# Kernel optimization log

Hardware: AMD Instinct MI355X
Metric: run time of the kernel (lower is better)

The kernel has to match this reference:

```python
import jax, jax.numpy as jnp
import numpy as np

N = 100000
F = 128
H = 128
E = 3200000


def setup_inputs() -> dict:
    key = jax.random.key(0)
    ks = jax.random.split(key, 12)
    s = 1.0 / np.sqrt(F)
    return {
        "x": jax.random.normal(ks[0], (N, F), jnp.float32),
        "edge_weight": jax.random.uniform(ks[1], (E,), jnp.float32),
        "p": jax.random.normal(ks[2], (F,), jnp.float32) * s,
        "w_ih": jax.random.normal(ks[3], (3 * F, F), jnp.float32) * s,
        "w_hh": jax.random.normal(ks[4], (3 * F, F), jnp.float32) * s,
        "b_ih": jax.random.normal(ks[5], (3 * F,), jnp.float32) * s,
        "b_hh": jax.random.normal(ks[6], (3 * F,), jnp.float32) * s,
        "w0": jax.random.normal(ks[7], (F, F), jnp.float32) * s,
        "w_lin": jax.random.normal(ks[8], (H, F), jnp.float32) * s,
        "b_lin": jax.random.normal(ks[9], (H,), jnp.float32) * s,
        "edge_index": jax.random.randint(ks[10], (2, E), 0, N, jnp.int64),
    }


def _evolve_gcnh(x, edge_index, edge_weight, p, w_ih, w_hh, b_ih, b_hh, w0):
    n_nodes, f = x.shape
    # --- TopKPooling: keep k = f nodes by learned projection score ---
    score = jnp.tanh((x @ p) / jnp.linalg.norm(p))  # [N]
    top_scores, idx = jax.lax.top_k(score, f)
    x_tilde = x[idx] * top_scores[:, None]  # [F, F]
    # --- single GRU step (batch=F, input=F): hidden state = GCN weight ---
    gi = x_tilde @ w_ih.T + b_ih  # [F, 3F]
    gh = w0 @ w_hh.T + b_hh       # [F, 3F]
    i_r, i_z, i_n = jnp.split(gi, 3, axis=-1)
    h_r, h_z, h_n = jnp.split(gh, 3, axis=-1)
    r = jax.nn.sigmoid(i_r + h_r)
    z = jax.nn.sigmoid(i_z + h_z)
    n = jnp.tanh(i_n + r * h_n)
    W = (1.0 - z) * n + z * w0  # evolved weight [F, F]
    # --- GCNConv with fixed W: sym-normalized sparse aggregation ---
    src, dst = edge_index[0], edge_index[1]
    loop = jnp.arange(n_nodes)
    src = jnp.concatenate([src, loop])
    dst = jnp.concatenate([dst, loop])
    ew = jnp.concatenate([edge_weight, jnp.ones((n_nodes,), x.dtype)])
    deg = jax.ops.segment_sum(ew, dst, num_segments=n_nodes)
    dinv = jnp.where(deg > 0, jax.lax.rsqrt(deg), 0.0)
    norm = dinv[src] * ew * dinv[dst]  # [E+N]
    xw = x @ W  # [N, F]
    out = jax.ops.segment_sum(norm[:, None] * xw[src], dst, num_segments=n_nodes)
    return out


def reference(x, edge_weight, p, w_ih, w_hh, b_ih, b_hh, w0, w_lin, b_lin, edge_index):
    h = _evolve_gcnh(x, edge_index, edge_weight, p, w_ih, w_hh, b_ih, b_hh, w0)
    h = jax.nn.relu(h)
    return h @ w_lin.T + b_lin
```

## Files before the change

kernel.cpp:

```cpp
#include <hip/hip_runtime.h>
#include <stdint.h>

#define FD 128
#define CAP 4096
#define PSH 8
#define NPART_MAX 512
#define NBLK1 256

static inline size_t alignup256(size_t x) { return (x + 255) & ~(size_t)255; }

struct EdgeP { int s; float w; };

typedef __attribute__((ext_vector_type(4))) float f32x4;
typedef __attribute__((ext_vector_type(8))) short bf16x8;

__device__ __forceinline__ unsigned short f32_to_bf16(float f) {
  unsigned u = __float_as_uint(f);
  u += 0x7fffu + ((u >> 16) & 1u);
  return (unsigned short)(u >> 16);
}
__device__ __forceinline__ float bf16lo(unsigned pair) {
  return __uint_as_float(pair << 16);
}
__device__ __forceinline__ float bf16hi(unsigned pair) {
  return __uint_as_float(pair & 0xffff0000u);
}
__device__ __forceinline__ unsigned pack_bf16(float a, float b) {
  return ((unsigned)f32_to_bf16(b) << 16) | (unsigned)f32_to_bf16(a);
}
__device__ __forceinline__ unsigned mono32(float f) {
  unsigned u = __float_as_uint(f);
  return (u & 0x80000000u) ? ~u : (u | 0x80000000u);
}
__device__ __forceinline__ unsigned long long mono64(double d) {
  unsigned long long b = (unsigned long long)__double_as_longlong(d);
  return (b & 0x8000000000000000ULL) ? ~b : (b | 0x8000000000000000ULL);
}

__global__ void score_pack(const float* __restrict__ x, const float* __restrict__ p,
                           double* __restrict__ dvals, unsigned* __restrict__ hist,
                           unsigned short* __restrict__ xb, unsigned* __restrict__ cnt, int N)
{
  int gid = blockIdx.x * blockDim.x + threadIdx.x;
  if (gid == 0) *cnt = 0u;
  int wid = gid >> 6, lane = threadIdx.x & 63;
  int nw = (gridDim.x * blockDim.x) >> 6;
  double p0 = (double)p[lane * 2], p1 = (double)p[lane * 2 + 1];
  for (int n = wid; n < N; n += nw) {
    float2 xv = *(const float2*)(x + (size_t)n * FD + lane * 2);
    unsigned pk = pack_bf16(xv.x, xv.y);
    *(unsigned*)(xb + (size_t)n * FD + lane * 2) = pk;
    double s = (double)xv.x * p0 + (double)xv.y * p1;
    #pragma unroll
    for (int o = 32; o > 0; o >>= 1) s += __shfl_down(s, o, 64);
    if (lane == 0) {
      dvals[n] = s;
      unsigned u = mono32((float)s);
      atomicAdd(&hist[u >> 16], 1u);
    }
  }
}

__global__ void find_thresh(const unsigned* __restrict__ hist, unsigned* __restrict__ Bthr)
{
  __shared__ unsigned part[1024];
  int t = threadIdx.x;
  unsigned s = 0;
  for (int i = 0; i < 64; i++) s += hist[t * 64 + i];
  part[t] = s;
  __syncthreads();
  if (t == 0) {
    unsigned cum = 0;
    int chunk = 1023;
    for (; chunk >= 0; chunk--) {
      if (cum + part[chunk] >= 128u) break;
      cum += part[chunk];
    }
    unsigned B = 0;
    if (chunk >= 0) {
      int b = chunk * 64 + 63;
      for (; b >= chunk * 64; b--) {
        cum += hist[b];
        if (cum >= 128u) break;
      }
      B = (unsigned)b;
    }
    *Bthr = B;
  }
}

__global__ void compact_kernel(const double* __restrict__ dvals, const unsigned* __restrict__ Bthr,
                               unsigned long long* __restrict__ ckey, unsigned* __restrict__ cidx,
                               unsigned* __restrict__ cnt, int N)
{
  int i = blockIdx.x * blockDim.x + threadIdx.x;
  if (i >= N) return;
  unsigned B = *Bthr;
  double d = dvals[i];
  unsigned u = mono32((float)d);
  if ((u >> 16) >= B) {
    unsigned pos = atomicAdd(cnt, 1u);
    if (pos < CAP) {
      ckey[pos] = ~mono64(d);
      cidx[pos] = (unsigned)i;
    }
  }
}

__global__ void topk_sort(const double* __restrict__ dvals, const float* __restrict__ p,
                          const unsigned* __restrict__ cnt,
                          const unsigned long long* __restrict__ ckey, const unsigned* __restrict__ cidx,
                          unsigned* __restrict__ sel_idx, float* __restrict__ sel_ts)
{
  __shared__ unsigned long long k[CAP];
  __shared__ unsigned id[CAP];
  __shared__ double red[128];
  __shared__ double pn_sh;
  int t = threadIdx.x;
  unsigned C = *cnt;
  if (C > CAP) C = CAP;
  int S = 128;
  while (S < (int)C) S <<= 1;
  for (int i = t; i < S; i += 1024) {
    if (i < (int)C) { k[i] = ckey[i]; id[i] = cidx[i]; }
    else            { k[i] = ~0ULL;   id[i] = 0xFFFFFFFFu; }
  }
  __syncthreads();
  for (int kk = 2; kk <= S; kk <<= 1) {
    for (int j = kk >> 1; j > 0; j >>= 1) {
      for (int i = t; i < S; i += 1024) {
        int q = i ^ j;
        if (q > i) {
          bool up = ((i & kk) == 0);
          bool g = (k[i] > k[q]) || (k[i] == k[q] && id[i] > id[q]);
          if (g == up) {
            unsigned long long tk = k[i]; k[i] = k[q]; k[q] = tk;
            unsigned ti = id[i]; id[i] = id[q]; id[q] = ti;
          }
        }
      }
      __syncthreads();
    }
  }
  if (t < 128) { double v = (double)p[t]; red[t] = v * v; }
  __syncthreads();
  if (t == 0) {
    double s = 0.0;
    for (int i = 0; i < 128; i++) s += red[i];
    pn_sh = sqrt(s);
  }
  __syncthreads();
  if (t < 128) {
    unsigned n = id[t];
    sel_idx[t] = n;
    sel_ts[t] = (float)tanh(dvals[n] / pn_sh);
  }
}

__global__ void transpose3(const float* __restrict__ w_ih, const float* __restrict__ w_hh,
                           const float* __restrict__ w_lin, float* __restrict__ w_ihT,
                           float* __restrict__ w_hhT, unsigned short* __restrict__ wlb)
{
  int b = blockIdx.x, c = threadIdx.x;
  if (b < 384)      w_ihT[(size_t)c * 384 + b]         = w_ih[(size_t)b * 128 + c];
  else if (b < 768) w_hhT[(size_t)c * 384 + (b - 384)] = w_hh[(size_t)(b - 384) * 128 + c];
  else              wlb[(size_t)(b - 768) * 128 + c]   = f32_to_bf16(w_lin[(size_t)(b - 768) * 128 + c]);
}

__global__ void gru_evolve(const float* __restrict__ x, const unsigned* __restrict__ sel_idx,
                           const float* __restrict__ sel_ts,
                           const float* __restrict__ w_ihT, const float* __restrict__ w_hhT,
                           const float* __restrict__ b_ih, const float* __restrict__ b_hh,
                           const float* __restrict__ w0, unsigned short* __restrict__ WbT)
{
  __shared__ float xt[FD], w0r[FD];
  int i = blockIdx.x, j = threadIdx.x;
  unsigned n = sel_idx[i];
  float ts = sel_ts[i];
  xt[j]  = x[(size_t)n * FD + j] * ts;
  w0r[j] = w0[i * FD + j];
  __syncthreads();
  float gir = b_ih[j], giz = b_ih[128 + j], gin = b_ih[256 + j];
  float ghr = b_hh[j], ghz = b_hh[128 + j], ghn = b_hh[256 + j];
  for (int kx = 0; kx < FD; kx++) {
    float xv = xt[kx], hv = w0r[kx];
    const float* wi = w_ihT + (size_t)kx * 384;
    const float* wh = w_hhT + (size_t)kx * 384;
    gir += xv * wi[j];
    giz += xv * wi[128 + j];
    gin += xv * wi[256 + j];
    ghr += hv * wh[j];
    ghz += hv * wh[128 + j];
    ghn += hv * wh[256 + j];
  }
  float r = 1.f / (1.f + expf(-(gir + ghr)));
  float z = 1.f / (1.f + expf(-(giz + ghz)));
  float nn = tanhf(gin + r * ghn);
  float wv = (1.f - z) * nn + z * w0r[j];
  WbT[(size_t)j * FD + i] = f32_to_bf16(wv);
}

__global__ __launch_bounds__(1024)
void part_count(const int* __restrict__ dstA, unsigned* __restrict__ cnt,
                int E, int NPART)
{
  __shared__ unsigned lh[NPART_MAX];
  for (int i = threadIdx.x; i < NPART; i += 1024) lh[i] = 0;
  __syncthreads();
  int chunk = (E + gridDim.x - 1) / gridDim.x;
  int e0 = blockIdx.x * chunk;
  int e1 = e0 + chunk; if (e1 > E) e1 = E;
  for (int e = e0 + threadIdx.x; e < e1; e += 1024)
    atomicAdd(&lh[dstA[e] >> PSH], 1u);
  __syncthreads();
  for (int i = threadIdx.x; i < NPART; i += 1024)
    cnt[(size_t)i * NBLK1 + blockIdx.x] = lh[i];
}

__global__ void scan_blocks(const unsigned* __restrict__ cnt, unsigned* __restrict__ basel,
                            unsigned* __restrict__ ptot)
{
  __shared__ unsigned s[NBLK1];
  int p = blockIdx.x, t = threadIdx.x;
  unsigned c = cnt[(size_t)p * NBLK1 + t];
  s[t] = c;
  __syncthreads();
  for (int ofs = 1; ofs < NBLK1; ofs <<= 1) {
    unsigned u = (t >= ofs) ? s[t - ofs] : 0u;
    __syncthreads();
    s[t] += u;
    __syncthreads();
  }
  basel[(size_t)p * NBLK1 + t] = s[t] - c;
  if (t == NBLK1 - 1) ptot[p] = s[t];
}

__global__ void scan_parts(const unsigned* __restrict__ ptot, int* __restrict__ poff,
                           int NPART, int E)
{
  __shared__ unsigned s[NPART_MAX];
  int t = threadIdx.x;
  unsigned c = (t < NPART) ? ptot[t] : 0u;
  s[t] = c;
  __syncthreads();
  for (int ofs = 1; ofs < NPART_MAX; ofs <<= 1) {
    unsigned u = (t >= ofs) ? s[t - ofs] : 0u;
    __syncthreads();
    s[t] += u;
    __syncthreads();
  }
  if (t < NPART) poff[t] = (int)(s[t] - c);
  if (t == 0) poff[NPART] = E;
}

__global__ __launch_bounds__(1024)
void part_place(const int* __restrict__ srcA, const int* __restrict__ dstA,
                const float* __restrict__ ew, const int* __restrict__ poff,
                const unsigned* __restrict__ basel,
                unsigned long long* __restrict__ epk2, int E, int NPART)
{
  __shared__ int lcur[NPART_MAX];
  int b = blockIdx.x;
  for (int i = threadIdx.x; i < NPART; i += 1024)
    lcur[i] = poff[i] + (int)basel[(size_t)i * NBLK1 + b];
  __syncthreads();
  int chunk = (E + gridDim.x - 1) / gridDim.x;
  int e0 = b * chunk;
  int e1 = e0 + chunk; if (e1 > E) e1 = E;
  for (int e = e0 + threadIdx.x; e < e1; e += 1024) {
    int d = dstA[e];
    int s = srcA[e];
    float w = ew[e];
    int p = d >> PSH;
    unsigned long long v = ((unsigned long long)__float_as_uint(w) << 32)
                         | ((unsigned long long)(unsigned)s << 8)
                         | (unsigned long long)(d & 255);
    int pos = atomicAdd(&lcur[p], 1);
    epk2[pos] = v;
  }
}

__global__ void part_csr(const int* __restrict__ poff, const unsigned long long* __restrict__ epk2,
                         EdgeP* __restrict__ epk_out, int* __restrict__ off,
                         float* __restrict__ dinv, int N, int NPART)
{
  int p = blockIdx.x;
  int beg = poff[p], end = poff[p + 1];
  int n0 = p << PSH;
  int nn = N - n0; if (nn > 256) nn = 256;
  __shared__ unsigned lcnt[256];
  __shared__ float ldeg[256];
  __shared__ unsigned lsc[256];
  int t = threadIdx.x;
  lcnt[t] = 0; ldeg[t] = 0.f;
  __syncthreads();
  for (int i = beg + t; i < end; i += 256) {
    unsigned long long v = epk2[i];
    int ln = (int)(v & 255u);
    float w = __uint_as_float((unsigned)(v >> 32));
    atomicAdd(&lcnt[ln], 1u);
    atomicAdd(&ldeg[ln], w);
  }
  __syncthreads();
  unsigned c = lcnt[t];
  lsc[t] = c;
  __syncthreads();
  for (int ofs = 1; ofs < 256; ofs <<= 1) {
    unsigned u = (t >= ofs) ? lsc[t - ofs] : 0u;
    __syncthreads();
    lsc[t] += u;
    __syncthreads();
  }
  unsigned excl = lsc[t] - c;
  if (t < nn) {
    off[n0 + t] = beg + (int)excl;
    dinv[n0 + t] = rsqrtf(ldeg[t] + 1.0f);
  }
  if (p == NPART - 1 && t == 0) off[N] = end;
  lcnt[t] = excl;
  __syncthreads();
  for (int i = beg + t; i < end; i += 256) {
    unsigned long long v = epk2[i];
    int ln = (int)(v & 255u);
    unsigned q = atomicAdd(&lcnt[ln], 1u);
    EdgeP ep;
    ep.s = (int)((v >> 8) & 0xFFFFFFu);
    ep.w = __uint_as_float((unsigned)(v >> 32));
    epk_out[beg + (int)q] = ep;
  }
}

__global__ __launch_bounds__(256)
void csr_gather4(const int* __restrict__ off, const EdgeP* __restrict__ epk,
                 const float* __restrict__ dinv, const unsigned short* __restrict__ xb,
                 unsigned short* __restrict__ aggb, int N)
{
  int gid = blockIdx.x * blockDim.x + threadIdx.x;
  int wid = gid >> 6, lane = threadIdx.x & 63;
  if (wid >= N) return;
  int g = lane >> 4, sub = lane & 15;
  int n = wid;
  int beg = off[n], end = off[n + 1];
  int cnt = end - beg;
  const EdgeP* ep_base = epk + beg;

  float di = dinv[n];
  uint4 xs4 = *(const uint4*)(xb + (size_t)n * FD + sub * 8);

  float acc[8];
  #pragma unroll
  for (int j = 0; j < 8; j++) acc[j] = 0.f;

  int nfull = cnt >> 4;
  int base = 0;
  for (int s16 = 0; s16 < nfull; s16++, base += 16) {
    uint2 ep[4];
    #pragma unroll
    for (int u = 0; u < 4; u++)
      ep[u] = *(const uint2*)(ep_base + base + u * 4 + g);
    float dv[4]; uint4 pv[4];
    #pragma unroll
    for (int u = 0; u < 4; u++) {
      int s = (int)ep[u].x;
      dv[u] = dinv[s];
      pv[u] = *(const uint4*)(xb + (size_t)s * FD + sub * 8);
    }
    #pragma unroll
    for (int u = 0; u < 4; u++) {
      float w = __uint_as_float(ep[u].y) * dv[u];
      acc[0] += w * bf16lo(pv[u].x); acc[1] += w * bf16hi(pv[u].x);
      acc[2] += w * bf16lo(pv[u].y); acc[3] += w * bf16hi(pv[u].y);
      acc[4] += w * bf16lo(pv[u].z); acc[5] += w * bf16hi(pv[u].z);
      acc[6] += w * bf16lo(pv[u].w); acc[7] += w * bf16hi(pv[u].w);
    }
  }
  if (base < cnt) {
    int last = cnt - 1;
    uint2 ep[4];
    #pragma unroll
    for (int u = 0; u < 4; u++) {
      int idx = base + u * 4 + g;
      int idc = idx < cnt ? idx : last;
      ep[u] = *(const uint2*)(ep_base + idc);
    }
    float dv[4]; uint4 pv[4];
    #pragma unroll
    for (int u = 0; u < 4; u++) {
      int s = (int)ep[u].x;
      dv[u] = dinv[s];
      pv[u] = *(const uint4*)(xb + (size_t)s * FD + sub * 8);
    }
    #pragma unroll
    for (int u = 0; u < 4; u++) {
      int idx = base + u * 4 + g;
      float w = (idx < cnt) ? __uint_as_float(ep[u].y) * dv[u] : 0.f;
      acc[0] += w * bf16lo(pv[u].x); acc[1] += w * bf16hi(pv[u].x);
      acc[2] += w * bf16lo(pv[u].y); acc[3] += w * bf16hi(pv[u].y);
      acc[4] += w * bf16lo(pv[u].z); acc[5] += w * bf16hi(pv[u].z);
      acc[6] += w * bf16lo(pv[u].w); acc[7] += w * bf16hi(pv[u].w);
    }
  }

  #pragma unroll
  for (int j = 0; j < 8; j++) {
    acc[j] += __shfl_xor(acc[j], 16, 64);
    acc[j] += __shfl_xor(acc[j], 32, 64);
  }
  if (g == 0) {
    float dii = di * di;
    uint4 o;
    o.x = pack_bf16(di * acc[0] + dii * bf16lo(xs4.x), di * acc[1] + dii * bf16hi(xs4.x));
    o.y = pack_bf16(di * acc[2] + dii * bf16lo(xs4.y), di * acc[3] + dii * bf16hi(xs4.y));
    o.z = pack_bf16(di * acc[4] + dii * bf16lo(xs4.z), di * acc[5] + dii * bf16hi(xs4.z));
    o.w = pack_bf16(di * acc[6] + dii * bf16lo(xs4.w), di * acc[7] + dii * bf16hi(xs4.w));
    *(uint4*)(aggb + (size_t)n * FD + sub * 8) = o;
  }
}

__global__ __launch_bounds__(256)
void gemm_mfma(const unsigned short* __restrict__ aggb, const unsigned short* __restrict__ WbT,
               const unsigned short* __restrict__ wlb, const float* __restrict__ bias,
               float* __restrict__ C, int nrows)
{
  __shared__ unsigned short hs[64][136];
  int tid = threadIdx.x;
  int wv = tid >> 6, lane = tid & 63;
  int row16 = lane & 15;
  int kgrp = lane >> 4;
  int r0 = blockIdx.x * 64;
  int arow = r0 + wv * 16 + row16;
  bool rowok = arow < nrows;

  f32x4 acc[8];
  #pragma unroll
  for (int t = 0; t < 8; t++) acc[t] = (f32x4){0.f, 0.f, 0.f, 0.f};

  #pragma unroll
  for (int ks = 0; ks < 4; ks++) {
    int k = ks * 32 + kgrp * 8;
    bf16x8 a;
    if (rowok) a = *(const bf16x8*)(aggb + (size_t)arow * FD + k);
    else       a = (bf16x8){0, 0, 0, 0, 0, 0, 0, 0};
    #pragma unroll
    for (int t = 0; t < 8; t++) {
      int col = t * 16 + row16;
      bf16x8 b = *(const bf16x8*)(WbT + (size_t)col * FD + k);
      acc[t] = __builtin_amdgcn_mfma_f32_16x16x32_bf16(a, b, acc[t], 0, 0, 0);
    }
  }
  #pragma unroll
  for (int t = 0; t < 8; t++) {
    int col = t * 16 + row16;
    #pragma unroll
    for (int r = 0; r < 4; r++) {
      int row_l = wv * 16 + kgrp * 4 + r;
      hs[row_l][col] = f32_to_bf16(fmaxf(acc[t][r], 0.f));
    }
  }
  __syncthreads();

  f32x4 acc2[8];
  #pragma unroll
  for (int t = 0; t < 8; t++) acc2[t] = (f32x4){0.f, 0.f, 0.f, 0.f};
  #pragma unroll
  for (int ks = 0; ks < 4; ks++) {
    int k = ks * 32 + kgrp * 8;
    bf16x8 a = *(const bf16x8*)(&hs[wv * 16 + row16][k]);
    #pragma unroll
    for (int t = 0; t < 8; t++) {
      int col = t * 16 + row16;
      bf16x8 b = *(const bf16x8*)(wlb + (size_t)col * FD + k);
      acc2[t] = __builtin_amdgcn_mfma_f32_16x16x32_bf16(a, b, acc2[t], 0, 0, 0);
    }
  }
  #pragma unroll
  for (int t = 0; t < 8; t++) {
    int col = t * 16 + row16;
    float bl = bias[col];
    #pragma unroll
    for (int r = 0; r < 4; r++) {
      int row = r0 + wv * 16 + kgrp * 4 + r;
      if (row < nrows) C[(size_t)row * FD + col] = acc2[t][r] + bl;
    }
  }
}

extern "C" void kernel_launch(void* const* d_in, const int* in_sizes, int n_in,
                              void* d_out, int out_size, void* d_ws, size_t ws_size,
                              hipStream_t stream)
{
  const float* x     = (const float*)d_in[0];
  const float* ew    = (const float*)d_in[1];
  const float* p     = (const float*)d_in[2];
  const float* w_ih  = (const float*)d_in[3];
  const float* w_hh  = (const float*)d_in[4];
  const float* b_ih  = (const float*)d_in[5];
  const float* b_hh  = (const float*)d_in[6];
  const float* w0    = (const float*)d_in[7];
  const float* w_lin = (const float*)d_in[8];
  const float* b_lin = (const float*)d_in[9];
  const int*   eidx  = (const int*)d_in[10];

  int N = in_sizes[0] / FD;
  int E = in_sizes[1];
  int NPART = (N + 255) >> PSH;
  const int* srcA = eidx;
  const int* dstA = eidx + E;

  char* base = (char*)d_ws;
  size_t off_ws = 0;
  auto take = [&](size_t bytes) -> void* {
    void* ptr = base + off_ws;
    off_ws = alignup256(off_ws + bytes);
    return ptr;
  };
  double* dvals = (double*)take((size_t)N * 8);
  unsigned* hist = (unsigned*)take(65536u * 4);
  unsigned* cnt = (unsigned*)take(4);
  unsigned* Bthr = (unsigned*)take(4);
  unsigned long long* ckey = (unsigned long long*)take((size_t)CAP * 8);
  unsigned* cidx = (unsigned*)take((size_t)CAP * 4);
  unsigned* sel_idx = (unsigned*)take(128 * 4);
  float* sel_ts = (float*)take(128 * 4);
  unsigned short* WbT = (unsigned short*)take(FD * FD * 2);
  unsigned short* wlb = (unsigned short*)take(FD * FD * 2);
  float* w_ihT = (float*)take(3 * FD * FD * 4);
  float* w_hhT = (float*)take(3 * FD * FD * 4);
  float* dinv = (float*)take((size_t)N * 4);
  unsigned* pcnt = (unsigned*)take((size_t)NPART_MAX * NBLK1 * 4);
  unsigned* basel = (unsigned*)take((size_t)NPART_MAX * NBLK1 * 4);
  unsigned* ptot = (unsigned*)take((size_t)NPART_MAX * 4);
  int* poff = (int*)take(((size_t)NPART_MAX + 1) * 4);
  int* off = (int*)take(((size_t)N + 1) * 4);
  unsigned long long* epk2 = (unsigned long long*)take((size_t)E * 8);
  EdgeP* epk_b = (EdgeP*)take((size_t)E * 8);
  unsigned short* xb = (unsigned short*)take((size_t)N * FD * 2);
  unsigned short* aggb = (unsigned short*)take((size_t)N * FD * 2);
  float* out1 = (float*)d_out;

  hipMemsetAsync(hist, 0, 65536u * 4, stream);

  score_pack<<<2048, 256, 0, stream>>>(x, p, dvals, hist, xb, cnt, N);
  find_thresh<<<1, 1024, 0, stream>>>(hist, Bthr);
  compact_kernel<<<(N + 255) / 256, 256, 0, stream>>>(dvals, Bthr, ckey, cidx, cnt, N);
  topk_sort<<<1, 1024, 0, stream>>>(dvals, p, cnt, ckey, cidx, sel_idx, sel_ts);
  transpose3<<<896, 128, 0, stream>>>(w_ih, w_hh, w_lin, w_ihT, w_hhT, wlb);
  gru_evolve<<<128, 128, 0, stream>>>(x, sel_idx, sel_ts, w_ihT, w_hhT, b_ih, b_hh, w0, WbT);

  part_count<<<NBLK1, 1024, 0, stream>>>(dstA, pcnt, E, NPART);
  scan_blocks<<<NPART, NBLK1, 0, stream>>>(pcnt, basel, ptot);
  scan_parts<<<1, NPART_MAX, 0, stream>>>(ptot, poff, NPART, E);
  part_place<<<NBLK1, 1024, 0, stream>>>(srcA, dstA, ew, poff, basel, epk2, E, NPART);
  part_csr<<<NPART, 256, 0, stream>>>(poff, epk2, epk_b, off, dinv, N, NPART);

  csr_gather4<<<(N * 64 + 255) / 256, 256, 0, stream>>>(off, epk_b, dinv, xb, aggb, N);
  gemm_mfma<<<(N + 63) / 64, 256, 0, stream>>>(aggb, WbT, wlb, b_lin, out1, N);
}
```

Measured before the change: 417.2 us.

## Build CSR with global per-node atomics instead of two-level partitioned sort

Replaces the partition-then-local-sort CSR build (block histograms, two scans, partition placement, per-partition local sort) with a direct approach. Per-node counts and weight sums come from global atomics, followed by a three-kernel prefix scan and edge placement through per-node atomic cursors. This removes one full pass over the edges and the intermediate epk2 buffer. In exchange it relies on heavily contended global atomics with scattered writes, and the order of edges within each node becomes nondeterministic.

Result: slower. 854.6 us (+104.9%).

```diff
diff --git a/kernel.cpp b/kernel.cpp
--- a/kernel.cpp
+++ b/kernel.cpp
@@ -3,9 +3,6 @@
 
 #define FD 128
 #define CAP 4096
-#define PSH 8
-#define NPART_MAX 512
-#define NBLK1 256
 
 static inline size_t alignup256(size_t x) { return (x + 255) & ~(size_t)255; }
 
@@ -200,134 +197,78 @@
   WbT[(size_t)j * FD + i] = f32_to_bf16(wv);
 }
 
+__global__ void deg_count(const int* __restrict__ dstA, const float* __restrict__ ew,
+                          unsigned* __restrict__ cntU, float* __restrict__ wsum, int E)
+{
+  int e = blockIdx.x * blockDim.x + threadIdx.x;
+  if (e >= E) return;
+  int d = dstA[e];
+  atomicAdd(&cntU[d], 1u);
+  atomicAdd(&wsum[d], ew[e]);
+}
+
 __global__ __launch_bounds__(1024)
-void part_count(const int* __restrict__ dstA, unsigned* __restrict__ cnt,
-                int E, int NPART)
-{
-  __shared__ unsigned lh[NPART_MAX];
-  for (int i = threadIdx.x; i < NPART; i += 1024) lh[i] = 0;
-  __syncthreads();
-  int chunk = (E + gridDim.x - 1) / gridDim.x;
-  int e0 = blockIdx.x * chunk;
-  int e1 = e0 + chunk; if (e1 > E) e1 = E;
-  for (int e = e0 + threadIdx.x; e < e1; e += 1024)
-    atomicAdd(&lh[dstA[e] >> PSH], 1u);
-  __syncthreads();
-  for (int i = threadIdx.x; i < NPART; i += 1024)
-    cnt[(size_t)i * NBLK1 + blockIdx.x] = lh[i];
-}
-
-__global__ void scan_blocks(const unsigned* __restrict__ cnt, unsigned* __restrict__ basel,
-                            unsigned* __restrict__ ptot)
-{
-  __shared__ unsigned s[NBLK1];
-  int p = blockIdx.x, t = threadIdx.x;
-  unsigned c = cnt[(size_t)p * NBLK1 + t];
+void scanA(const unsigned* __restrict__ cntU, unsigned* __restrict__ inblk,
+           unsigned* __restrict__ bsum, int N)
+{
+  __shared__ unsigned s[1024];
+  int b = blockIdx.x, t = threadIdx.x;
+  int i = b * 1024 + t;
+  unsigned c = (i < N) ? cntU[i] : 0u;
   s[t] = c;
   __syncthreads();
-  for (int ofs = 1; ofs < NBLK1; ofs <<= 1) {
+  for (int ofs = 1; ofs < 1024; ofs <<= 1) {
     unsigned u = (t >= ofs) ? s[t - ofs] : 0u;
     __syncthreads();
     s[t] += u;
     __syncthreads();
   }
-  basel[(size_t)p * NBLK1 + t] = s[t] - c;
-  if (t == NBLK1 - 1) ptot[p] = s[t];
-}
-
-__global__ void scan_parts(const unsigned* __restrict__ ptot, int* __restrict__ poff,
-                           int NPART, int E)
-{
-  __shared__ unsigned s[NPART_MAX];
+  if (i < N) inblk[i] = s[t] - c;
+  if (t == 1023) bsum[b] = s[t];
+}
+
+__global__ __launch_bounds__(1024)
+void scanB(unsigned* __restrict__ bsum, int NB)
+{
+  __shared__ unsigned s[1024];
   int t = threadIdx.x;
-  unsigned c = (t < NPART) ? ptot[t] : 0u;
+  unsigned c = (t < NB) ? bsum[t] : 0u;
   s[t] = c;
   __syncthreads();
-  for (int ofs = 1; ofs < NPART_MAX; ofs <<= 1) {
+  for (int ofs = 1; ofs < 1024; ofs <<= 1) {
     unsigned u = (t >= ofs) ? s[t - ofs] : 0u;
     __syncthreads();
     s[t] += u;
     __syncthreads();
   }
-  if (t < NPART) poff[t] = (int)(s[t] - c);
-  if (t == 0) poff[NPART] = E;
-}
-
-__global__ __launch_bounds__(1024)
-void part_place(const int* __restrict__ srcA, const int* __restrict__ dstA,
-                const float* __restrict__ ew, const int* __restrict__ poff,
-                const unsigned* __restrict__ basel,
-                unsigned long long* __restrict__ epk2, int E, int NPART)
-{
-  __shared__ int lcur[NPART_MAX];
-  int b = blockIdx.x;
-  for (int i = threadIdx.x; i < NPART; i += 1024)
-    lcur[i] = poff[i] + (int)basel[(size_t)i * NBLK1 + b];
-  __syncthreads();
-  int chunk = (E + gridDim.x - 1) / gridDim.x;
-  int e0 = b * chunk;
-  int e1 = e0 + chunk; if (e1 > E) e1 = E;
-  for (int e = e0 + threadIdx.x; e < e1; e += 1024) {
-    int d = dstA[e];
-    int s = srcA[e];
-    float w = ew[e];
-    int p = d >> PSH;
-    unsigned long long v = ((unsigned long long)__float_as_uint(w) << 32)
-                         | ((unsigned long long)(unsigned)s << 8)
-                         | (unsigned long long)(d & 255);
-    int pos = atomicAdd(&lcur[p], 1);
-    epk2[pos] = v;
-  }
-}
-
-__global__ void part_csr(const int* __restrict__ poff, const unsigned long long* __restrict__ epk2,
-                         EdgeP* __restrict__ epk_out, int* __restrict__ off,
-                         float* __restrict__ dinv, int N, int NPART)
-{
-  int p = blockIdx.x;
-  int beg = poff[p], end = poff[p + 1];
-  int n0 = p << PSH;
-  int nn = N - n0; if (nn > 256) nn = 256;
-  __shared__ unsigned lcnt[256];
-  __shared__ float ldeg[256];
-  __shared__ unsigned lsc[256];
-  int t = threadIdx.x;
-  lcnt[t] = 0; ldeg[t] = 0.f;
-  __syncthreads();
-  for (int i = beg + t; i < end; i += 256) {
-    unsigned long long v = epk2[i];
-    int ln = (int)(v & 255u);
-    float w = __uint_as_float((unsigned)(v >> 32));
-    atomicAdd(&lcnt[ln], 1u);
-    atomicAdd(&ldeg[ln], w);
-  }
-  __syncthreads();
-  unsigned c = lcnt[t];
-  lsc[t] = c;
-  __syncthreads();
-  for (int ofs = 1; ofs < 256; ofs <<= 1) {
-    unsigned u = (t >= ofs) ? lsc[t - ofs] : 0u;
-    __syncthreads();
-    lsc[t] += u;
-    __syncthreads();
-  }
-  unsigned excl = lsc[t] - c;
-  if (t < nn) {
-    off[n0 + t] = beg + (int)excl;
-    dinv[n0 + t] = rsqrtf(ldeg[t] + 1.0f);
-  }
-  if (p == NPART - 1 && t == 0) off[N] = end;
-  lcnt[t] = excl;
-  __syncthreads();
-  for (int i = beg + t; i < end; i += 256) {
-    unsigned long long v = epk2[i];
-    int ln = (int)(v & 255u);
-    unsigned q = atomicAdd(&lcnt[ln], 1u);
-    EdgeP ep;
-    ep.s = (int)((v >> 8) & 0xFFFFFFu);
-    ep.w = __uint_as_float((unsigned)(v >> 32));
-    epk_out[beg + (int)q] = ep;
-  }
+  if (t < NB) bsum[t] = s[t] - c;
+}
+
+__global__ void scanC(const unsigned* __restrict__ inblk, const unsigned* __restrict__ bsum,
+                      const float* __restrict__ wsum, int* __restrict__ off,
+                      int* __restrict__ cur, float* __restrict__ dinv, int N, int E)
+{
+  int i = blockIdx.x * blockDim.x + threadIdx.x;
+  if (i < N) {
+    int o = (int)(inblk[i] + bsum[i >> 10]);
+    off[i] = o;
+    cur[i] = o;
+    dinv[i] = rsqrtf(wsum[i] + 1.0f);
+  }
+  if (i == 0) off[N] = E;
+}
+
+__global__ void place_edges(const int* __restrict__ srcA, const int* __restrict__ dstA,
+                            const float* __restrict__ ew, int* __restrict__ cur,
+                            unsigned long long* __restrict__ epk, int E)
+{
+  int e = blockIdx.x * blockDim.x + threadIdx.x;
+  if (e >= E) return;
+  int d = dstA[e];
+  int s = srcA[e];
+  float w = ew[e];
+  int pos = atomicAdd(&cur[d], 1);
+  epk[pos] = ((unsigned long long)__float_as_uint(w) << 32) | (unsigned)s;
 }
 
 __global__ __launch_bounds__(256)
@@ -503,7 +444,6 @@
 
   int N = in_sizes[0] / FD;
   int E = in_sizes[1];
-  int NPART = (N + 255) >> PSH;
   const int* srcA = eidx;
   const int* dstA = eidx + E;
 
@@ -527,18 +467,21 @@
   float* w_ihT = (float*)take(3 * FD * FD * 4);
   float* w_hhT = (float*)take(3 * FD * FD * 4);
   float* dinv = (float*)take((size_t)N * 4);
-  unsigned* pcnt = (unsigned*)take((size_t)NPART_MAX * NBLK1 * 4);
-  unsigned* basel = (unsigned*)take((size_t)NPART_MAX * NBLK1 * 4);
-  unsigned* ptot = (unsigned*)take((size_t)NPART_MAX * 4);
-  int* poff = (int*)take(((size_t)NPART_MAX + 1) * 4);
+  unsigned* cntU = (unsigned*)take((size_t)N * 8);
+  float* wsum = (float*)(cntU + N);
+  unsigned* inblk = (unsigned*)take((size_t)N * 4);
+  unsigned* bsum = (unsigned*)take(1024 * 4);
+  int* cur = (int*)take((size_t)N * 4);
   int* off = (int*)take(((size_t)N + 1) * 4);
-  unsigned long long* epk2 = (unsigned long long*)take((size_t)E * 8);
   EdgeP* epk_b = (EdgeP*)take((size_t)E * 8);
   unsigned short* xb = (unsigned short*)take((size_t)N * FD * 2);
   unsigned short* aggb = (unsigned short*)take((size_t)N * FD * 2);
   float* out1 = (float*)d_out;
 
+  int NB = (N + 1023) / 1024;
+
   hipMemsetAsync(hist, 0, 65536u * 4, stream);
+  hipMemsetAsync(cntU, 0, (size_t)N * 8, stream);
 
   score_pack<<<2048, 256, 0, stream>>>(x, p, dvals, hist, xb, cnt, N);
   find_thresh<<<1, 1024, 0, stream>>>(hist, Bthr);
@@ -547,11 +490,12 @@
   transpose3<<<896, 128, 0, stream>>>(w_ih, w_hh, w_lin, w_ihT, w_hhT, wlb);
   gru_evolve<<<128, 128, 0, stream>>>(x, sel_idx, sel_ts, w_ihT, w_hhT, b_ih, b_hh, w0, WbT);
 
-  part_count<<<NBLK1, 1024, 0, stream>>>(dstA, pcnt, E, NPART);
-  scan_blocks<<<NPART, NBLK1, 0, stream>>>(pcnt, basel, ptot);
-  scan_parts<<<1, NPART_MAX, 0, stream>>>(ptot, poff, NPART, E);
-  part_place<<<NBLK1, 1024, 0, stream>>>(srcA, dstA, ew, poff, basel, epk2, E, NPART);
-  part_csr<<<NPART, 256, 0, stream>>>(poff, epk2, epk_b, off, dinv, N, NPART);
+  deg_count<<<(E + 255) / 256, 256, 0, stream>>>(dstA, ew, cntU, wsum, E);
+  scanA<<<NB, 1024, 0, stream>>>(cntU, inblk, bsum, N);
+  scanB<<<1, 1024, 0, stream>>>(bsum, NB);
+  scanC<<<(N + 255) / 256, 256, 0, stream>>>(inblk, bsum, wsum, off, cur, dinv, N, E);
+  place_edges<<<(E + 255) / 256, 256, 0, stream>>>(srcA, dstA, ew, cur,
+                                                   (unsigned long long*)epk_b, E);
 
   csr_gather4<<<(N * 64 + 255) / 256, 256, 0, stream>>>(off, epk_b, dinv, xb, aggb, N);
   gemm_mfma<<<(N + 63) / 64, 256, 0, stream>>>(aggb, WbT, wlb, b_lin, out1, N);
```

## Stage partitioned edges in shared memory before coalesced global scatter

Applied to the files above, without the earlier changes.

The partition-place kernel now buffers each block's edges in LDS, sorted by partition through a local histogram and scan. It then writes them out contiguously per partition, so global stores to the edge array become runs rather than scattered single writes. The block count rises to 1024 with 512 threads each so every chunk (~3125 edges) fits in the 4096-entry LDS buffer. This adds an extra pass over dstA, a local scan and a binary search per output element. The scan_blocks kernel now runs 1024-thread blocks to match.

New measurement: 404.6 us. -3.0%, faster.

```diff
diff --git a/kernel.cpp b/kernel.cpp
--- a/kernel.cpp
+++ b/kernel.cpp
@@ -5,7 +5,8 @@
 #define CAP 4096
 #define PSH 8
 #define NPART_MAX 512
-#define NBLK1 256
+#define NBLK1 1024
+#define EBUF_MAX 4096
 
 static inline size_t alignup256(size_t x) { return (x + 255) & ~(size_t)255; }
 
@@ -217,8 +218,9 @@
     cnt[(size_t)i * NBLK1 + blockIdx.x] = lh[i];
 }
 
-__global__ void scan_blocks(const unsigned* __restrict__ cnt, unsigned* __restrict__ basel,
-                            unsigned* __restrict__ ptot)
+__global__ __launch_bounds__(1024)
+void scan_blocks(const unsigned* __restrict__ cnt, unsigned* __restrict__ basel,
+                 unsigned* __restrict__ ptot)
 {
   __shared__ unsigned s[NBLK1];
   int p = blockIdx.x, t = threadIdx.x;
@@ -253,21 +255,43 @@
   if (t == 0) poff[NPART] = E;
 }
 
-__global__ __launch_bounds__(1024)
+__global__ __launch_bounds__(512)
 void part_place(const int* __restrict__ srcA, const int* __restrict__ dstA,
                 const float* __restrict__ ew, const int* __restrict__ poff,
                 const unsigned* __restrict__ basel,
                 unsigned long long* __restrict__ epk2, int E, int NPART)
 {
-  __shared__ int lcur[NPART_MAX];
-  int b = blockIdx.x;
-  for (int i = threadIdx.x; i < NPART; i += 1024)
-    lcur[i] = poff[i] + (int)basel[(size_t)i * NBLK1 + b];
-  __syncthreads();
+  __shared__ unsigned long long ebuf[EBUF_MAX];
+  __shared__ unsigned lcnt[NPART_MAX];
+  __shared__ unsigned lsc[NPART_MAX];
+  __shared__ unsigned lbase[NPART_MAX + 1];
+  __shared__ unsigned cur[NPART_MAX];
+  __shared__ int gbase[NPART_MAX];
+  int b = blockIdx.x, t = threadIdx.x;
   int chunk = (E + gridDim.x - 1) / gridDim.x;
   int e0 = b * chunk;
   int e1 = e0 + chunk; if (e1 > E) e1 = E;
-  for (int e = e0 + threadIdx.x; e < e1; e += 1024) {
+  int n = e1 - e0;
+
+  lcnt[t] = 0;
+  __syncthreads();
+  for (int e = e0 + t; e < e1; e += 512)
+    atomicAdd(&lcnt[dstA[e] >> PSH], 1u);
+  __syncthreads();
+  lsc[t] = lcnt[t];
+  __syncthreads();
+  for (int ofs = 1; ofs < NPART_MAX; ofs <<= 1) {
+    unsigned u = (t >= ofs) ? lsc[t - ofs] : 0u;
+    __syncthreads();
+    lsc[t] += u;
+    __syncthreads();
+  }
+  lbase[t] = lsc[t] - lcnt[t];
+  if (t == NPART_MAX - 1) lbase[NPART_MAX] = lsc[t];
+  cur[t] = lsc[t] - lcnt[t];
+  gbase[t] = (t < NPART) ? (poff[t] + (int)basel[(size_t)t * NBLK1 + b]) : 0;
+  __syncthreads();
+  for (int e = e0 + t; e < e1; e += 512) {
     int d = dstA[e];
     int s = srcA[e];
     float w = ew[e];
@@ -275,8 +299,17 @@
     unsigned long long v = ((unsigned long long)__float_as_uint(w) << 32)
                          | ((unsigned long long)(unsigned)s << 8)
                          | (unsigned long long)(d & 255);
-    int pos = atomicAdd(&lcur[p], 1);
-    epk2[pos] = v;
+    unsigned pos = atomicAdd(&cur[p], 1u);
+    ebuf[pos] = v;
+  }
+  __syncthreads();
+  for (int j = t; j < n; j += 512) {
+    int lo = 0, hi = NPART_MAX;
+    while (hi - lo > 1) {
+      int mid = (lo + hi) >> 1;
+      if (lbase[mid] <= (unsigned)j) lo = mid; else hi = mid;
+    }
+    epk2[gbase[lo] + (j - (int)lbase[lo])] = ebuf[j];
   }
 }
 
@@ -550,7 +583,7 @@
   part_count<<<NBLK1, 1024, 0, stream>>>(dstA, pcnt, E, NPART);
   scan_blocks<<<NPART, NBLK1, 0, stream>>>(pcnt, basel, ptot);
   scan_parts<<<1, NPART_MAX, 0, stream>>>(ptot, poff, NPART, E);
-  part_place<<<NBLK1, 1024, 0, stream>>>(srcA, dstA, ew, poff, basel, epk2, E, NPART);
+  part_place<<<NBLK1, 512, 0, stream>>>(srcA, dstA, ew, poff, basel, epk2, E, NPART);
   part_csr<<<NPART, 256, 0, stream>>>(poff, epk2, epk_b, off, dinv, N, NPART);
 
   csr_gather4<<<(N * 64 + 255) / 256, 256, 0, stream>>>(off, epk_b, dinv, xb, aggb, N);
```
